# Kernel tuning notes

Measured on AMD Instinct MI355X. Metric: run time of the kernel, lower is better.

The kernel has to match this reference:

```python
import jax, jax.numpy as jnp
import numpy as np

N = 500000   # total nodes in batched graph
B = 8192     # number of graphs
H = 128      # hidden_dim
L = 3        # num_layer -> feature_dim F = H*L = 384
F = H * L
S2S_STEPS = 3
VOCAB = 143


def setup_inputs() -> dict:
    key = jax.random.key(0)
    ks = jax.random.split(key, 12)
    sc = 0.02
    unit_type = jax.random.randint(ks[0], (N,), 0, VOCAB)
    # sorted segment ids covering every graph (contiguous, all B segments non-empty)
    node2graph = (jnp.arange(N) * B) // N
    return {
        'unit_type': unit_type,
        'node2graph': node2graph,
        'embed':    jax.random.normal(ks[1], (VOCAB, H)) * sc,
        'msg_W1':   jax.random.normal(ks[2], (H, 2 * H)) * sc,
        'msg_b1':   jnp.zeros((H,)),
        'msg_W2':   jax.random.normal(ks[3], (H, H)) * sc,
        'msg_b2':   jnp.zeros((H,)),
        'gru_Wih':  jax.random.normal(ks[4], (3 * H, H)) * sc,
        'gru_Whh':  jax.random.normal(ks[5], (3 * H, H)) * sc,
        'gru_bih':  jnp.zeros((3 * H,)),
        'gru_bhh':  jnp.zeros((3 * H,)),
        'lstm_Wih': jax.random.normal(ks[6], (4 * F, 2 * F)) * sc,
        'lstm_Whh': jax.random.normal(ks[7], (4 * F, F)) * sc,
        'lstm_bih': jnp.zeros((4 * F,)),
        'lstm_bhh': jnp.zeros((4 * F,)),
    }


def _gru_step(x, h, Wih, Whh, bih, bhh):
    # single-timestep PyTorch GRU cell; gate order r, z, n
    gi = x @ Wih.T + bih
    gh = h @ Whh.T + bhh
    ir, iz, inn = jnp.split(gi, 3, axis=-1)
    hr, hz, hn = jnp.split(gh, 3, axis=-1)
    r = jax.nn.sigmoid(ir + hr)
    z = jax.nn.sigmoid(iz + hz)
    n = jnp.tanh(inn + r * hn)
    return (1.0 - z) * n + z * h


def _lstm_step(x, h, c, Wih, Whh, bih, bhh):
    # single-timestep PyTorch LSTM cell; gate order i, f, g, o
    g = x @ Wih.T + bih + h @ Whh.T + bhh
    i, f, gc, o = jnp.split(g, 4, axis=-1)
    c = jax.nn.sigmoid(f) * c + jax.nn.sigmoid(i) * jnp.tanh(gc)
    h = jax.nn.sigmoid(o) * jnp.tanh(c)
    return h, c


def reference(unit_type, node2graph, embed, msg_W1, msg_b1, msg_W2, msg_b2,
              gru_Wih, gru_Whh, gru_bih, gru_bhh,
              lstm_Wih, lstm_Whh, lstm_bih, lstm_bhh):
    # --- node update stack ---
    layer_input = embed[unit_type]          # [N, H]
    hx = layer_input                        # GRU hidden state (1 layer)
    hiddens = []
    for _ in range(L):
        x2 = jnp.concatenate([layer_input, layer_input], axis=-1)   # [N, 2H]
        msg = jnp.maximum(x2 @ msg_W1.T + msg_b1, 0.0) @ msg_W2.T + msg_b2
        hx = _gru_step(msg, hx, gru_Wih, gru_Whh, gru_bih, gru_bhh)
        hiddens.append(hx)
        layer_input = hx
    node_feature = jnp.concatenate(hiddens, axis=-1)                # [N, F]

    # --- Set2Set readout ---
    h = jnp.zeros((B, F), dtype=node_feature.dtype)
    c = jnp.zeros((B, F), dtype=node_feature.dtype)
    q_star = jnp.zeros((B, 2 * F), dtype=node_feature.dtype)
    for _ in range(S2S_STEPS):
        h, c = _lstm_step(q_star, h, c, lstm_Wih, lstm_Whh, lstm_bih, lstm_bhh)
        q = h                                                       # [B, F]
        logits = jnp.sum(q[node2graph] * node_feature, axis=-1)     # [N]
        m = jax.ops.segment_max(logits, node2graph, num_segments=B,
                                indices_are_sorted=True)
        e = jnp.exp(logits - m[node2graph])
        z = jax.ops.segment_sum(e, node2graph, num_segments=B,
                                indices_are_sorted=True)
        att = e / z[node2graph]                                     # [N]
        pooled = jax.ops.segment_sum(att[:, None] * node_feature, node2graph,
                                     num_segments=B, indices_are_sorted=True)
        q_star = jnp.concatenate([q, pooled], axis=-1)              # [B, 2F]

    return q_star, node_feature
```

## Files before the change

kernel.cpp:

```cpp
#include <hip/hip_runtime.h>

typedef unsigned short u16;
typedef unsigned int   u32;
typedef u16 bfx8 __attribute__((ext_vector_type(8)));
typedef __bf16 bf16x8 __attribute__((ext_vector_type(8)));
typedef float  f32x4  __attribute__((ext_vector_type(4)));

#define NH  128
#define NF  384
#define K2F 768
#define NG4 1536

__device__ __forceinline__ float bf2f(u16 u){ return __uint_as_float(((u32)u) << 16); }
__device__ __forceinline__ u16 f2bf(float f){
  __bf16 h = (__bf16)f;
  return __builtin_bit_cast(u16, h);
}
__device__ __forceinline__ float fsig(float x){ return 1.0f / (1.0f + __expf(-x)); }
__device__ __forceinline__ float ftanh(float x){ return 1.0f - 2.0f / (__expf(2.0f * x) + 1.0f); }

struct P {
  const int *unit_type, *n2g;
  const void *embed, *w1, *b1, *w2, *b2, *gwih, *gwhh, *gbih, *gbhh, *lwih, *lwhh, *lbih, *lbhh;
  int *flag, *segS, *segE;
  u16 *embedB;
  u16 *W1eb, *W2b, *Wihb, *Whhb;
  float *b1f, *b2f, *bihG, *bhhG;
  u16 *WcatB;
  float *bsum;
  float *h1v, *c1v;
  float *hbuf, *cbuf, *pooled;
  u16 *xcatB;
  float *gout;
  u16 *nfb;
  int useNfb;
  void *out; long qsz;
  int N, B, embedN;
};

__device__ __forceinline__ float ldin(const void* p, long i, int isbf){
  return isbf ? bf2f(((const u16*)p)[i]) : ((const float*)p)[i];
}

__global__ void k_detect(P p){
  __shared__ int cnt;
  if (threadIdx.x == 0) cnt = 0;
  __syncthreads();
  const u32* w = (const u32*)p.embed;
  const int nw = p.embedN / 2;
  int bad = 0;
  for (int i = threadIdx.x; i < nw; i += blockDim.x){
    u32 v = w[i];
    float fhi = __uint_as_float(v & 0xffff0000u);
    float flo = __uint_as_float(v << 16);
    if (!(fabsf(fhi) < 2.0f)) bad++;
    if (!(fabsf(flo) < 2.0f)) bad++;
  }
  atomicAdd(&cnt, bad);
  __syncthreads();
  if (threadIdx.x == 0) *p.flag = (cnt == 0) ? 1 : 0;
}

__global__ void k_prep(P p){
  long o = (long)blockIdx.x * 256 + threadIdx.x;
  const int isbf = *p.flag;
  if (o < p.embedN){ p.embedB[o] = f2bf(ldin(p.embed, o, isbf)); return; } o -= p.embedN;
  if (o < 16384){ long cc = o >> 7, k = o & 127;
    float v = ldin(p.w1, cc*256 + k, isbf) + ldin(p.w1, cc*256 + 128 + k, isbf);
    p.W1eb[o] = f2bf(v); return; } o -= 16384;
  if (o < 16384){ p.W2b[o]  = f2bf(ldin(p.w2, o, isbf));   return; } o -= 16384;
  if (o < 49152){ p.Wihb[o] = f2bf(ldin(p.gwih, o, isbf)); return; } o -= 49152;
  if (o < 49152){ p.Whhb[o] = f2bf(ldin(p.gwhh, o, isbf)); return; } o -= 49152;
  if (o < (long)NG4*K2F){ long j = o / K2F, k = o - j*K2F;
    float v = ldin(p.lwih, o, isbf);
    if (k < NF) v += ldin(p.lwhh, j*NF + k, isbf);
    p.WcatB[o] = f2bf(v); return; } o -= (long)NG4*K2F;
  if (o < NH){ p.b1f[o] = ldin(p.b1, o, isbf); return; } o -= NH;
  if (o < NH){ p.b2f[o] = ldin(p.b2, o, isbf); return; } o -= NH;
  if (o < NF){ p.bihG[o] = ldin(p.gbih, o, isbf); return; } o -= NF;
  if (o < NF){ p.bhhG[o] = ldin(p.gbhh, o, isbf); return; } o -= NF;
  if (o < NG4){ p.bsum[o] = ldin(p.lbih, o, isbf) + ldin(p.lbhh, o, isbf); return; } o -= NG4;
  if (o < p.B){ p.segS[o] = 0; p.segE[o] = 0; }
}

__global__ void k_segb(P p){
  int i = (int)blockIdx.x * 256 + threadIdx.x;
  if (i >= p.N) return;
  int g = p.n2g[i];
  if (g < 0 || g >= p.B) return;
  if (i == 0        || p.n2g[i-1] != g) p.segS[g] = i;
  if (i == p.N - 1  || p.n2g[i+1] != g) p.segE[g] = i + 1;
}

__device__ __forceinline__ f32x4 MF(bf16x8 a, bf16x8 b, f32x4 c){
  return __builtin_amdgcn_mfma_f32_16x16x32_bf16(a, b, c, 0, 0, 0);
}
__device__ __forceinline__ bf16x8 ldA(const u16* buf, int m0, int k0, int lane){
  const int row = m0 + (lane & 15);
  const int byte = (row*256 + (k0 + (lane>>4)*8)*2) ^ ((row&7)<<4);
  return *(const bf16x8*)((const char*)buf + byte);
}
__device__ __forceinline__ bf16x8 ldB(const u16* __restrict__ W, int n0, int k0, int lane){
  return *(const bf16x8*)(W + (long)(n0 + (lane&15))*NH + k0 + (lane>>4)*8);
}
__device__ __forceinline__ bf16x8 ldBs(const u16* __restrict__ W, long stride,
                                       int n0, int k0, int lane){
  return *(const bf16x8*)(W + (long)(n0 + (lane&15))*stride + k0 + (lane>>4)*8);
}
__device__ __forceinline__ void stLDS(u16* buf, int row, int col, float v){
  const int byte = (row*256 + col*2) ^ ((row&7)<<4);
  *(u16*)((char*)buf + byte) = f2bf(v);
}
__device__ __forceinline__ float ldLDS(const u16* buf, int row, int col){
  const int byte = (row*256 + col*2) ^ ((row&7)<<4);
  return bf2f(*(const u16*)((const char*)buf + byte));
}
__device__ __forceinline__ u16 ldLDSraw(const u16* buf, int row, int col){
  const int byte = (row*256 + col*2) ^ ((row&7)<<4);
  return *(const u16*)((const char*)buf + byte);
}

__global__ __launch_bounds__(256, 3) void k_stageA_mfma(P p){
  __shared__ u16 hA[64*128];
  __shared__ u16 mA[64*128];
  __shared__ u16 gA[64*128];
  const int t = (int)threadIdx.x;
  const int lane = t & 63, w = t >> 6;
  const int node0 = (int)blockIdx.x * 64;
  const int cL = lane & 15;
  const int isbf = *p.flag;

  {
    const int row = t >> 2, seg = t & 3;
    const int node = min(node0 + row, p.N - 1);
    int ut = p.unit_type[node];
    ut = min(max(ut, 0), p.embedN/NH - 1);
    const u16* src = p.embedB + (long)ut*NH + seg*32;
    #pragma unroll
    for (int i = 0; i < 4; ++i){
      const int col = seg*32 + i*8;
      const int byte = (row*256 + col*2) ^ ((row&7)<<4);
      *(bfx8*)((char*)hA + byte) = *(const bfx8*)(src + i*8);
    }
  }
  __syncthreads();

  u16*   out16 = (u16*)p.out;
  float* out32 = (float*)p.out;

  #pragma unroll 1
  for (int l = 0; l < 3; ++l){
    {
      f32x4 acc[2][4];
      #pragma unroll
      for (int nt = 0; nt < 2; ++nt){
        const float b = p.b1f[w*32 + nt*16 + cL];
        #pragma unroll
        for (int m = 0; m < 4; ++m) acc[nt][m] = {b,b,b,b};
      }
      for (int k0 = 0; k0 < 128; k0 += 32){
        bf16x8 bv[2];
        #pragma unroll
        for (int nt = 0; nt < 2; ++nt) bv[nt] = ldB(p.W1eb, w*32 + nt*16, k0, lane);
        bf16x8 a[4];
        #pragma unroll
        for (int m = 0; m < 4; ++m) a[m] = ldA(hA, m*16, k0, lane);
        #pragma unroll
        for (int nt = 0; nt < 2; ++nt)
          #pragma unroll
          for (int m = 0; m < 4; ++m) acc[nt][m] = MF(a[m], bv[nt], acc[nt][m]);
      }
      #pragma unroll
      for (int nt = 0; nt < 2; ++nt)
        #pragma unroll
        for (int m = 0; m < 4; ++m)
          #pragma unroll
          for (int j = 0; j < 4; ++j)
            stLDS(mA, m*16 + (lane>>4)*4 + j, w*32 + nt*16 + cL,
                  fmaxf(acc[nt][m][j], 0.0f));
    }
    __syncthreads();
    {
      f32x4 acc[2][4];
      #pragma unroll
      for (int nt = 0; nt < 2; ++nt){
        const float b = p.b2f[w*32 + nt*16 + cL];
        #pragma unroll
        for (int m = 0; m < 4; ++m) acc[nt][m] = {b,b,b,b};
      }
      for (int k0 = 0; k0 < 128; k0 += 32){
        bf16x8 bv[2];
        #pragma unroll
        for (int nt = 0; nt < 2; ++nt) bv[nt] = ldB(p.W2b, w*32 + nt*16, k0, lane);
        bf16x8 a[4];
        #pragma unroll
        for (int m = 0; m < 4; ++m) a[m] = ldA(mA, m*16, k0, lane);
        #pragma unroll
        for (int nt = 0; nt < 2; ++nt)
          #pragma unroll
          for (int m = 0; m < 4; ++m) acc[nt][m] = MF(a[m], bv[nt], acc[nt][m]);
      }
      __syncthreads();
      #pragma unroll
      for (int nt = 0; nt < 2; ++nt)
        #pragma unroll
        for (int m = 0; m < 4; ++m)
          #pragma unroll
          for (int j = 0; j < 4; ++j)
            stLDS(gA, m*16 + (lane>>4)*4 + j, w*32 + nt*16 + cL, acc[nt][m][j]);
    }
    __syncthreads();
    f32x4 rr[2][4];
    {
      f32x4 acc[4][4];
      #pragma unroll
      for (int tc = 0; tc < 4; ++tc){
        const int col = (tc < 2 ? 0 : 128) + w*32 + (tc&1)*16 + cL;
        const float b = p.bihG[col] + p.bhhG[col];
        #pragma unroll
        for (int m = 0; m < 4; ++m) acc[tc][m] = {b,b,b,b};
      }
      for (int k0 = 0; k0 < 128; k0 += 32){
        bf16x8 bv[4];
        #pragma unroll
        for (int tc = 0; tc < 4; ++tc)
          bv[tc] = ldB(p.Wihb, (tc < 2 ? 0 : 128) + w*32 + (tc&1)*16, k0, lane);
        bf16x8 a[4];
        #pragma unroll
        for (int m = 0; m < 4; ++m) a[m] = ldA(gA, m*16, k0, lane);
        #pragma unroll
        for (int tc = 0; tc < 4; ++tc)
          #pragma unroll
          for (int m = 0; m < 4; ++m) acc[tc][m] = MF(a[m], bv[tc], acc[tc][m]);
      }
      for (int k0 = 0; k0 < 128; k0 += 32){
        bf16x8 bv[4];
        #pragma unroll
        for (int tc = 0; tc < 4; ++tc)
          bv[tc] = ldB(p.Whhb, (tc < 2 ? 0 : 128) + w*32 + (tc&1)*16, k0, lane);
        bf16x8 a[4];
        #pragma unroll
        for (int m = 0; m < 4; ++m) a[m] = ldA(hA, m*16, k0, lane);
        #pragma unroll
        for (int tc = 0; tc < 4; ++tc)
          #pragma unroll
          for (int m = 0; m < 4; ++m) acc[tc][m] = MF(a[m], bv[tc], acc[tc][m]);
      }
      #pragma unroll
      for (int nt = 0; nt < 2; ++nt)
        #pragma unroll
        for (int m = 0; m < 4; ++m)
          #pragma unroll
          for (int j = 0; j < 4; ++j){
            rr[nt][m][j] = fsig(acc[nt][m][j]);
            stLDS(mA, m*16 + (lane>>4)*4 + j, w*32 + nt*16 + cL,
                  fsig(acc[nt+2][m][j]));
          }
    }
    {
      f32x4 inn[2][4], hnn[2][4];
      #pragma unroll
      for (int nt = 0; nt < 2; ++nt){
        const int col = 256 + w*32 + nt*16 + cL;
        const float bi = p.bihG[col], bh = p.bhhG[col];
        #pragma unroll
        for (int m = 0; m < 4; ++m){ inn[nt][m] = {bi,bi,bi,bi}; hnn[nt][m] = {bh,bh,bh,bh}; }
      }
      for (int k0 = 0; k0 < 128; k0 += 32){
        bf16x8 bv[2];
        #pragma unroll
        for (int nt = 0; nt < 2; ++nt) bv[nt] = ldB(p.Wihb, 256 + w*32 + nt*16, k0, lane);
        bf16x8 a[4];
        #pragma unroll
        for (int m = 0; m < 4; ++m) a[m] = ldA(gA, m*16, k0, lane);
        #pragma unroll
        for (int nt = 0; nt < 2; ++nt)
          #pragma unroll
          for (int m = 0; m < 4; ++m) inn[nt][m] = MF(a[m], bv[nt], inn[nt][m]);
      }
      for (int k0 = 0; k0 < 128; k0 += 32){
        bf16x8 bv[2];
        #pragma unroll
        for (int nt = 0; nt < 2; ++nt) bv[nt] = ldB(p.Whhb, 256 + w*32 + nt*16, k0, lane);
        bf16x8 a[4];
        #pragma unroll
        for (int m = 0; m < 4; ++m) a[m] = ldA(hA, m*16, k0, lane);
        #pragma unroll
        for (int nt = 0; nt < 2; ++nt)
          #pragma unroll
          for (int m = 0; m < 4; ++m) hnn[nt][m] = MF(a[m], bv[nt], hnn[nt][m]);
      }
      #pragma unroll
      for (int nt = 0; nt < 2; ++nt)
        #pragma unroll
        for (int m = 0; m < 4; ++m)
          #pragma unroll
          for (int j = 0; j < 4; ++j){
            const int row = m*16 + (lane>>4)*4 + j;
            const int col = w*32 + nt*16 + cL;
            const float nn = ftanh(fmaf(rr[nt][m][j], hnn[nt][m][j], inn[nt][m][j]));
            const float zv = ldLDS(mA, row, col);
            const float hv = ldLDS(hA, row, col);
            inn[nt][m][j] = fmaf(zv, hv - nn, nn);
          }
      __syncthreads();
      #pragma unroll
      for (int nt = 0; nt < 2; ++nt)
        #pragma unroll
        for (int m = 0; m < 4; ++m)
          #pragma unroll
          for (int j = 0; j < 4; ++j)
            stLDS(hA, m*16 + (lane>>4)*4 + j, w*32 + nt*16 + cL, inn[nt][m][j]);
      __syncthreads();
    }
    {
      const int col = t & 127;
      const int rh  = t >> 7;
      #pragma unroll 4
      for (int rb = 0; rb < 64; rb += 2){
        const int row = rb + rh;
        const int node = node0 + row;
        if (node < p.N){
          const u16 hv16 = ldLDSraw(hA, row, col);
          const long fi = (long)node*NF + l*NH + col;
          if (isbf){
            __builtin_nontemporal_store(hv16, &out16[p.qsz + fi]);
          } else {
            __builtin_nontemporal_store(bf2f(hv16), &out32[p.qsz + fi]);
            if (p.useNfb) __builtin_nontemporal_store(hv16, &p.nfb[fi]);
          }
        }
      }
    }
  }
}

__global__ void k_lstm0(P p){
  const int d = (int)threadIdx.x;
  if (d >= NF) return;
  const float i_ = fsig(p.bsum[d]);
  const float gc = ftanh(p.bsum[2*NF + d]);
  const float o_ = fsig(p.bsum[3*NF + d]);
  const float cn = i_ * gc;
  p.c1v[d] = cn;
  p.h1v[d] = o_ * ftanh(cn);
}

__global__ __launch_bounds__(256) void k_attn(P p, const float* __restrict__ qsrc,
                                              int qstride, int finalstep){
  __shared__ alignas(16) char raw[32 * NF * 4];
  __shared__ float qs[NF];
  __shared__ float att[32];
  __shared__ float sM, sZ, sSc;

  u16*   nb = (u16*)raw;
  float* nfl = (float*)raw;
  const int t = (int)threadIdx.x;
  const int g = (int)blockIdx.x;
  const int isbf = *p.flag;
  const int bftile = isbf | p.useNfb;
  const u16* nbase = isbf ? (const u16*)p.out + p.qsz : p.nfb;
  const float* o32 = (const float*)p.out;

  for (int i = t; i < NF; i += 256) qs[i] = qsrc[(long)g*qstride + i];
  if (t == 0){ sM = -1e30f; sZ = 0.0f; sSc = 1.0f; }
  int n0 = p.segS[g], n1 = p.segE[g];
  n0 = max(n0, 0); n1 = min(n1, p.N);
  float acc0 = 0.f, acc1 = 0.f;
  __syncthreads();

  for (int base = n0; base < n1; base += 32){
    const int cnt = min(32, n1 - base);
    {
      const int i = t >> 3, q8 = t & 7;
      if (i < cnt){
        if (bftile){
          const bfx8* src = (const bfx8*)(nbase + (long)(base + i)*NF + q8*48);
          #pragma unroll
          for (int j8 = 0; j8 < 6; ++j8)
            *(bfx8*)&nb[i*NF + q8*48 + j8*8] = __builtin_nontemporal_load(src + j8);
        } else {
          const f32x4* src = (const f32x4*)(o32 + p.qsz + (long)(base + i)*NF + q8*48);
          #pragma unroll
          for (int j4 = 0; j4 < 12; ++j4)
            *(f32x4*)&nfl[i*NF + q8*48 + j4*4] = __builtin_nontemporal_load(src + j4);
        }
      }
    }
    __syncthreads();
    {
      const int w = t >> 6, lane = t & 63;
      for (int ii = w; ii < cnt; ii += 4){
        float dot = 0.f;
        #pragma unroll
        for (int j = 0; j < 6; ++j){
          const int d = lane + 64*j;
          const float v = bftile ? bf2f(nb[ii*NF + d]) : nfl[ii*NF + d];
          dot = fmaf(v, qs[d], dot);
        }
        #pragma unroll
        for (int off = 32; off; off >>= 1) dot += __shfl_xor(dot, off);
        if (lane == 0) att[ii] = dot;
      }
    }
    __syncthreads();
    if (t < 32){
      const float l = (t < cnt) ? att[t] : -1e30f;
      float m = l;
      #pragma unroll
      for (int off = 16; off; off >>= 1) m = fmaxf(m, __shfl_xor(m, off));
      const float mnew = fmaxf(sM, m);
      const float e = (t < cnt) ? __expf(l - mnew) : 0.f;
      float z = e;
      #pragma unroll
      for (int off = 16; off; off >>= 1) z += __shfl_xor(z, off);
      if (t < cnt) att[t] = e;
      if (t == 0){
        const float sc = __expf(sM - mnew);
        sSc = sc; sZ = sZ * sc + z; sM = mnew;
      }
    }
    __syncthreads();
    {
      const float sc = sSc;
      acc0 *= sc; acc1 *= sc;
      for (int ii = 0; ii < cnt; ++ii){
        const float a = att[ii];
        const float v0 = bftile ? bf2f(nb[ii*NF + t]) : nfl[ii*NF + t];
        acc0 = fmaf(a, v0, acc0);
        if (t < 128){
          const float v1 = bftile ? bf2f(nb[ii*NF + 256 + t]) : nfl[ii*NF + 256 + t];
          acc1 = fmaf(a, v1, acc1);
        }
      }
    }
    __syncthreads();
  }

  const float invZ = (sZ != 0.0f) ? 1.0f / sZ : 0.0f;
  const float p0 = acc0 * invZ, p1 = acc1 * invZ;
  p.pooled[(long)g*NF + t] = p0;
  if (t < 128) p.pooled[(long)g*NF + 256 + t] = p1;
  if (finalstep){
    const long rb = (long)g * K2F;
    if (isbf){
      u16* o = (u16*)p.out;
      o[rb + t] = f2bf(qs[t]);
      if (t < 128) o[rb + 256 + t] = f2bf(qs[256 + t]);
      o[rb + NF + t] = f2bf(p0);
      if (t < 128) o[rb + NF + 256 + t] = f2bf(p1);
    } else {
      float* o = (float*)p.out;
      o[rb + t] = qs[t];
      if (t < 128) o[rb + 256 + t] = qs[256 + t];
      o[rb + NF + t] = p0;
      if (t < 128) o[rb + NF + 256 + t] = p1;
    }
  }
}

__global__ void k_xcat(P p, const float* __restrict__ hsrc, int hstride){
  const int d2 = (int)blockIdx.x * 256 + threadIdx.x;
  const int g  = (int)blockIdx.y;
  if (d2 >= K2F) return;
  const float v = (d2 < NF) ? hsrc[(long)g*hstride + d2]
                            : p.pooled[(long)g*NF + d2 - NF];
  p.xcatB[(long)g*K2F + d2] = f2bf(v);
}

__global__ __launch_bounds__(256, 4) void k_gemm_mfma(P p){
  __shared__ u16 aT[64*128];
  const int t = (int)threadIdx.x;
  const int lane = t & 63, w = t >> 6, cL = lane & 15;
  const int row0 = (int)blockIdx.x * 64, col0 = (int)blockIdx.y * 128;

  f32x4 acc[2][4];
  #pragma unroll
  for (int nt = 0; nt < 2; ++nt)
    #pragma unroll
    for (int m = 0; m < 4; ++m) acc[nt][m] = {0.f,0.f,0.f,0.f};

  for (int kc = 0; kc < K2F; kc += 128){
    __syncthreads();
    {
      const int row = t >> 2, seg = t & 3;
      const int gr = row0 + row;
      const u16* src = p.xcatB + (long)gr*K2F + kc + seg*32;
      #pragma unroll
      for (int i = 0; i < 4; ++i){
        const int col = seg*32 + i*8;
        const int byte = (row*256 + col*2) ^ ((row&7)<<4);
        bfx8 v = {0,0,0,0,0,0,0,0};
        if (gr < p.B) v = *(const bfx8*)(src + i*8);
        *(bfx8*)((char*)aT + byte) = v;
      }
    }
    __syncthreads();
    for (int k0 = 0; k0 < 128; k0 += 32){
      bf16x8 bv[2];
      #pragma unroll
      for (int nt = 0; nt < 2; ++nt)
        bv[nt] = ldBs(p.WcatB, K2F, col0 + w*32 + nt*16, kc + k0, lane);
      bf16x8 a[4];
      #pragma unroll
      for (int m = 0; m < 4; ++m) a[m] = ldA(aT, m*16, k0, lane);
      #pragma unroll
      for (int nt = 0; nt < 2; ++nt)
        #pragma unroll
        for (int m = 0; m < 4; ++m) acc[nt][m] = MF(a[m], bv[nt], acc[nt][m]);
    }
  }
  #pragma unroll
  for (int nt = 0; nt < 2; ++nt){
    const int col = col0 + w*32 + nt*16 + cL;
    const float bs = p.bsum[col];
    #pragma unroll
    for (int m = 0; m < 4; ++m)
      #pragma unroll
      for (int j = 0; j < 4; ++j){
        const int row = row0 + m*16 + (lane>>4)*4 + j;
        if (row < p.B) p.gout[(long)row*NG4 + col] = acc[nt][m][j] + bs;
      }
  }
}

__global__ void k_gates(P p, const float* __restrict__ csrc, int cstride){
  const long idx = (long)blockIdx.x * 256 + threadIdx.x;
  if (idx >= (long)p.B * NF) return;
  const int g = (int)(idx / NF), d = (int)(idx - (long)g*NF);
  const float* gr = p.gout + (long)g*NG4;
  const float i_ = fsig(gr[d]);
  const float f_ = fsig(gr[NF + d]);
  const float gc = ftanh(gr[2*NF + d]);
  const float o_ = fsig(gr[3*NF + d]);
  const float cp = csrc[(long)g*cstride + d];
  const float cn = fmaf(f_, cp, i_ * gc);
  p.cbuf[(long)g*NF + d] = cn;
  p.hbuf[(long)g*NF + d] = o_ * ftanh(cn);
}

extern "C" void kernel_launch(void* const* d_in, const int* in_sizes, int n_in,
                              void* d_out, int out_size, void* d_ws, size_t ws_size,
                              hipStream_t stream){
  P p{};
  p.unit_type = (const int*)d_in[0];
  p.n2g  = (const int*)d_in[1];
  p.embed = d_in[2];  p.w1 = d_in[3];  p.b1 = d_in[4];  p.w2 = d_in[5];  p.b2 = d_in[6];
  p.gwih = d_in[7];  p.gwhh = d_in[8]; p.gbih = d_in[9]; p.gbhh = d_in[10];
  p.lwih = d_in[11]; p.lwhh = d_in[12]; p.lbih = d_in[13]; p.lbhh = d_in[14];

  const int N = in_sizes[0];
  const int B = (int)(((long)out_size - (long)N*NF) / K2F);
  p.N = N; p.B = B; p.embedN = in_sizes[2];
  p.out = d_out; p.qsz = (long)B * K2F;

  char* w = (char*)d_ws;
  size_t used = 0;
  auto alloc = [&](size_t bytes) -> char* {
    char* r = w + used;
    used += (bytes + 255) & ~(size_t)255;
    return r;
  };
  p.flag  = (int*)alloc(4);
  p.segS  = (int*)alloc((size_t)B*4);
  p.segE  = (int*)alloc((size_t)B*4);
  p.embedB= (u16*)  alloc((size_t)p.embedN*2);
  p.W1eb  = (u16*)  alloc(16384*2);
  p.W2b   = (u16*)  alloc(16384*2);
  p.Wihb  = (u16*)  alloc(49152*2);
  p.Whhb  = (u16*)  alloc(49152*2);
  p.b1f   = (float*)alloc(NH*4);
  p.b2f   = (float*)alloc(NH*4);
  p.bihG  = (float*)alloc(NF*4);
  p.bhhG  = (float*)alloc(NF*4);
  p.WcatB = (u16*)  alloc((size_t)NG4*K2F*2);
  p.bsum  = (float*)alloc(NG4*4);
  p.h1v   = (float*)alloc(NF*4);
  p.c1v   = (float*)alloc(NF*4);
  p.hbuf  = (float*)alloc((size_t)B*NF*4);
  p.cbuf  = (float*)alloc((size_t)B*NF*4);
  p.pooled= (float*)alloc((size_t)B*NF*4);
  p.xcatB = (u16*)  alloc((size_t)B*K2F*2);
  p.gout  = (float*)alloc((size_t)B*NG4*4);
  if (used > ws_size){
    (void)hipMemsetAsync(d_out, 0, (size_t)out_size * 2, stream);
    return;
  }
  const size_t nfbBytes = (size_t)N * NF * 2;
  if (used + nfbBytes + 256 <= ws_size){
    p.nfb = (u16*)alloc(nfbBytes);
    p.useNfb = 1;
  } else {
    p.nfb = (u16*)p.flag;
    p.useNfb = 0;
  }

  const long prepTot = (long)p.embedN + 16384 + 16384 + 49152 + 49152
                     + (long)NG4*K2F + NH + NH + NF + NF + NG4 + B;

  k_detect<<<1, 256, 0, stream>>>(p);
  k_prep  <<<(int)((prepTot + 255)/256), 256, 0, stream>>>(p);
  k_segb  <<<(N + 255)/256, 256, 0, stream>>>(p);
  k_stageA_mfma<<<(N + 63)/64, 256, 0, stream>>>(p);
  k_lstm0 <<<1, NF, 0, stream>>>(p);

  const dim3 gemmG((B + 63)/64, NG4/128);
  k_attn <<<B, 256, 0, stream>>>(p, p.h1v, 0, 0);
  k_xcat <<<dim3(3, B), 256, 0, stream>>>(p, p.h1v, 0);
  k_gemm_mfma<<<gemmG, 256, 0, stream>>>(p);
  k_gates<<<(int)(((long)B*NF + 255)/256), 256, 0, stream>>>(p, p.c1v, 0);
  k_attn <<<B, 256, 0, stream>>>(p, p.hbuf, NF, 0);
  k_xcat <<<dim3(3, B), 256, 0, stream>>>(p, p.hbuf, NF);
  k_gemm_mfma<<<gemmG, 256, 0, stream>>>(p);
  k_gates<<<(int)(((long)B*NF + 255)/256), 256, 0, stream>>>(p, p.cbuf, NF);
  k_attn <<<B, 256, 0, stream>>>(p, p.hbuf, NF, 1);
}
```

Measured before the change: 1.994 ms.

## Give each wave its own 16-row slab and fuse GRU gates without block syncs

Stage A is reorganised so that each wave owns 16 node rows and computes all 128 output columns of every matmul. The A fragments stay in registers, so no block-wide __syncthreads are needed. The GRU r/z/n gate matmuls and their elementwise update are fused into one per-column-tile loop, and the two LDS buffers ping-pong across layers, cutting LDS from 48KB to 32KB per block. In exchange, every wave now fetches the full weight matrices (four times the weight traffic per block), and the column-tile loops are not unrolled, which shortens the independent MFMA chains.

```diff
diff --git a/kernel.cpp b/kernel.cpp
--- a/kernel.cpp
+++ b/kernel.cpp
@@ -121,17 +121,21 @@
 }
 
 __global__ __launch_bounds__(256, 3) void k_stageA_mfma(P p){
-  __shared__ u16 hA[64*128];
-  __shared__ u16 mA[64*128];
-  __shared__ u16 gA[64*128];
+  __shared__ u16 bufA[64*128];
+  __shared__ u16 bufB[64*128];
   const int t = (int)threadIdx.x;
   const int lane = t & 63, w = t >> 6;
   const int node0 = (int)blockIdx.x * 64;
+  const int r0 = w * 16;
   const int cL = lane & 15;
   const int isbf = *p.flag;
 
+  u16* bufH = bufA;
+  u16* bufM = bufB;
+
   {
-    const int row = t >> 2, seg = t & 3;
+    const int row = r0 + (lane >> 2);
+    const int seg = lane & 3;
     const int node = min(node0 + row, p.N - 1);
     int ut = p.unit_type[node];
     ut = min(max(ut, 0), p.embedN/NH - 1);
@@ -140,198 +144,107 @@
     for (int i = 0; i < 4; ++i){
       const int col = seg*32 + i*8;
       const int byte = (row*256 + col*2) ^ ((row&7)<<4);
-      *(bfx8*)((char*)hA + byte) = *(const bfx8*)(src + i*8);
-    }
-  }
-  __syncthreads();
+      *(bfx8*)((char*)bufH + byte) = *(const bfx8*)(src + i*8);
+    }
+  }
 
   u16*   out16 = (u16*)p.out;
   float* out32 = (float*)p.out;
 
   #pragma unroll 1
   for (int l = 0; l < 3; ++l){
+    bf16x8 ah[4];
+    #pragma unroll
+    for (int k = 0; k < 4; ++k) ah[k] = ldA(bufH, r0, k*32, lane);
+
+    #pragma unroll 1
+    for (int ct = 0; ct < 8; ++ct){
+      const float b = p.b1f[ct*16 + cL];
+      f32x4 acc = {b,b,b,b};
+      #pragma unroll
+      for (int k = 0; k < 4; ++k){
+        const bf16x8 bv = ldB(p.W1eb, ct*16, k*32, lane);
+        acc = MF(ah[k], bv, acc);
+      }
+      #pragma unroll
+      for (int j = 0; j < 4; ++j)
+        stLDS(bufM, r0 + (lane>>4)*4 + j, ct*16 + cL, fmaxf(acc[j], 0.0f));
+    }
     {
-      f32x4 acc[2][4];
-      #pragma unroll
-      for (int nt = 0; nt < 2; ++nt){
-        const float b = p.b1f[w*32 + nt*16 + cL];
-        #pragma unroll
-        for (int m = 0; m < 4; ++m) acc[nt][m] = {b,b,b,b};
-      }
-      for (int k0 = 0; k0 < 128; k0 += 32){
-        bf16x8 bv[2];
-        #pragma unroll
-        for (int nt = 0; nt < 2; ++nt) bv[nt] = ldB(p.W1eb, w*32 + nt*16, k0, lane);
-        bf16x8 a[4];
-        #pragma unroll
-        for (int m = 0; m < 4; ++m) a[m] = ldA(hA, m*16, k0, lane);
-        #pragma unroll
-        for (int nt = 0; nt < 2; ++nt)
-          #pragma unroll
-          for (int m = 0; m < 4; ++m) acc[nt][m] = MF(a[m], bv[nt], acc[nt][m]);
-      }
-      #pragma unroll
-      for (int nt = 0; nt < 2; ++nt)
-        #pragma unroll
-        for (int m = 0; m < 4; ++m)
-          #pragma unroll
-          for (int j = 0; j < 4; ++j)
-            stLDS(mA, m*16 + (lane>>4)*4 + j, w*32 + nt*16 + cL,
-                  fmaxf(acc[nt][m][j], 0.0f));
-    }
-    __syncthreads();
+      bf16x8 am[4];
+      #pragma unroll
+      for (int k = 0; k < 4; ++k) am[k] = ldA(bufM, r0, k*32, lane);
+      #pragma unroll 1
+      for (int ct = 0; ct < 8; ++ct){
+        const float b = p.b2f[ct*16 + cL];
+        f32x4 acc = {b,b,b,b};
+        #pragma unroll
+        for (int k = 0; k < 4; ++k){
+          const bf16x8 bv = ldB(p.W2b, ct*16, k*32, lane);
+          acc = MF(am[k], bv, acc);
+        }
+        #pragma unroll
+        for (int j = 0; j < 4; ++j)
+          stLDS(bufM, r0 + (lane>>4)*4 + j, ct*16 + cL, acc[j]);
+      }
+    }
     {
-      f32x4 acc[2][4];
-      #pragma unroll
-      for (int nt = 0; nt < 2; ++nt){
-        const float b = p.b2f[w*32 + nt*16 + cL];
-        #pragma unroll
-        for (int m = 0; m < 4; ++m) acc[nt][m] = {b,b,b,b};
-      }
-      for (int k0 = 0; k0 < 128; k0 += 32){
-        bf16x8 bv[2];
-        #pragma unroll
-        for (int nt = 0; nt < 2; ++nt) bv[nt] = ldB(p.W2b, w*32 + nt*16, k0, lane);
-        bf16x8 a[4];
-        #pragma unroll
-        for (int m = 0; m < 4; ++m) a[m] = ldA(mA, m*16, k0, lane);
-        #pragma unroll
-        for (int nt = 0; nt < 2; ++nt)
-          #pragma unroll
-          for (int m = 0; m < 4; ++m) acc[nt][m] = MF(a[m], bv[nt], acc[nt][m]);
-      }
-      __syncthreads();
-      #pragma unroll
-      for (int nt = 0; nt < 2; ++nt)
-        #pragma unroll
-        for (int m = 0; m < 4; ++m)
-          #pragma unroll
-          for (int j = 0; j < 4; ++j)
-            stLDS(gA, m*16 + (lane>>4)*4 + j, w*32 + nt*16 + cL, acc[nt][m][j]);
-    }
-    __syncthreads();
-    f32x4 rr[2][4];
-    {
-      f32x4 acc[4][4];
-      #pragma unroll
-      for (int tc = 0; tc < 4; ++tc){
-        const int col = (tc < 2 ? 0 : 128) + w*32 + (tc&1)*16 + cL;
-        const float b = p.bihG[col] + p.bhhG[col];
-        #pragma unroll
-        for (int m = 0; m < 4; ++m) acc[tc][m] = {b,b,b,b};
-      }
-      for (int k0 = 0; k0 < 128; k0 += 32){
-        bf16x8 bv[4];
-        #pragma unroll
-        for (int tc = 0; tc < 4; ++tc)
-          bv[tc] = ldB(p.Wihb, (tc < 2 ? 0 : 128) + w*32 + (tc&1)*16, k0, lane);
-        bf16x8 a[4];
-        #pragma unroll
-        for (int m = 0; m < 4; ++m) a[m] = ldA(gA, m*16, k0, lane);
-        #pragma unroll
-        for (int tc = 0; tc < 4; ++tc)
-          #pragma unroll
-          for (int m = 0; m < 4; ++m) acc[tc][m] = MF(a[m], bv[tc], acc[tc][m]);
-      }
-      for (int k0 = 0; k0 < 128; k0 += 32){
-        bf16x8 bv[4];
-        #pragma unroll
-        for (int tc = 0; tc < 4; ++tc)
-          bv[tc] = ldB(p.Whhb, (tc < 2 ? 0 : 128) + w*32 + (tc&1)*16, k0, lane);
-        bf16x8 a[4];
-        #pragma unroll
-        for (int m = 0; m < 4; ++m) a[m] = ldA(hA, m*16, k0, lane);
-        #pragma unroll
-        for (int tc = 0; tc < 4; ++tc)
-          #pragma unroll
-          for (int m = 0; m < 4; ++m) acc[tc][m] = MF(a[m], bv[tc], acc[tc][m]);
-      }
-      #pragma unroll
-      for (int nt = 0; nt < 2; ++nt)
-        #pragma unroll
-        for (int m = 0; m < 4; ++m)
-          #pragma unroll
-          for (int j = 0; j < 4; ++j){
-            rr[nt][m][j] = fsig(acc[nt][m][j]);
-            stLDS(mA, m*16 + (lane>>4)*4 + j, w*32 + nt*16 + cL,
-                  fsig(acc[nt+2][m][j]));
+      bf16x8 am[4];
+      #pragma unroll
+      for (int k = 0; k < 4; ++k) am[k] = ldA(bufM, r0, k*32, lane);
+      #pragma unroll 1
+      for (int ct = 0; ct < 8; ++ct){
+        const int c16 = ct*16 + cL;
+        const float br = p.bihG[c16]       + p.bhhG[c16];
+        const float bz = p.bihG[128 + c16] + p.bhhG[128 + c16];
+        const float bi = p.bihG[256 + c16];
+        const float bh = p.bhhG[256 + c16];
+        f32x4 ar = {br,br,br,br}, az = {bz,bz,bz,bz};
+        f32x4 ai = {bi,bi,bi,bi}, an = {bh,bh,bh,bh};
+        #pragma unroll
+        for (int k = 0; k < 4; ++k){
+          bf16x8 bv;
+          bv = ldB(p.Wihb,       ct*16, k*32, lane); ar = MF(am[k], bv, ar);
+          bv = ldB(p.Whhb,       ct*16, k*32, lane); ar = MF(ah[k], bv, ar);
+          bv = ldB(p.Wihb, 128 + ct*16, k*32, lane); az = MF(am[k], bv, az);
+          bv = ldB(p.Whhb, 128 + ct*16, k*32, lane); az = MF(ah[k], bv, az);
+          bv = ldB(p.Wihb, 256 + ct*16, k*32, lane); ai = MF(am[k], bv, ai);
+          bv = ldB(p.Whhb, 256 + ct*16, k*32, lane); an = MF(ah[k], bv, an);
+        }
+        #pragma unroll
+        for (int j = 0; j < 4; ++j){
+          const int row = r0 + (lane>>4)*4 + j;
+          const int col = ct*16 + cL;
+          const float r = fsig(ar[j]);
+          const float z = fsig(az[j]);
+          const float nn = ftanh(fmaf(r, an[j], ai[j]));
+          const float hv = ldLDS(bufH, row, col);
+          stLDS(bufM, row, col, fmaf(z, hv - nn, nn));
+        }
+      }
+    }
+    #pragma unroll 1
+    for (int rj = 0; rj < 16; ++rj){
+      const int row = r0 + rj;
+      const int node = node0 + row;
+      if (node < p.N){
+        const u16 va = ldLDSraw(bufM, row, lane);
+        const u16 vb = ldLDSraw(bufM, row, 64 + lane);
+        const long fi = (long)node*NF + l*NH;
+        if (isbf){
+          __builtin_nontemporal_store(va, &out16[p.qsz + fi + lane]);
+          __builtin_nontemporal_store(vb, &out16[p.qsz + fi + 64 + lane]);
+        } else {
+          __builtin_nontemporal_store(bf2f(va), &out32[p.qsz + fi + lane]);
+          __builtin_nontemporal_store(bf2f(vb), &out32[p.qsz + fi + 64 + lane]);
+          if (p.useNfb){
+            __builtin_nontemporal_store(va, &p.nfb[fi + lane]);
+            __builtin_nontemporal_store(vb, &p.nfb[fi + 64 + lane]);
           }
-    }
-    {
-      f32x4 inn[2][4], hnn[2][4];
-      #pragma unroll
-      for (int nt = 0; nt < 2; ++nt){
-        const int col = 256 + w*32 + nt*16 + cL;
-        const float bi = p.bihG[col], bh = p.bhhG[col];
-        #pragma unroll
-        for (int m = 0; m < 4; ++m){ inn[nt][m] = {bi,bi,bi,bi}; hnn[nt][m] = {bh,bh,bh,bh}; }
-      }
-      for (int k0 = 0; k0 < 128; k0 += 32){
-        bf16x8 bv[2];
-        #pragma unroll
-        for (int nt = 0; nt < 2; ++nt) bv[nt] = ldB(p.Wihb, 256 + w*32 + nt*16, k0, lane);
-        bf16x8 a[4];
-        #pragma unroll
-        for (int m = 0; m < 4; ++m) a[m] = ldA(gA, m*16, k0, lane);
-        #pragma unroll
-        for (int nt = 0; nt < 2; ++nt)
-          #pragma unroll
-          for (int m = 0; m < 4; ++m) inn[nt][m] = MF(a[m], bv[nt], inn[nt][m]);
-      }
-      for (int k0 = 0; k0 < 128; k0 += 32){
-        bf16x8 bv[2];
-        #pragma unroll
-        for (int nt = 0; nt < 2; ++nt) bv[nt] = ldB(p.Whhb, 256 + w*32 + nt*16, k0, lane);
-        bf16x8 a[4];
-        #pragma unroll
-        for (int m = 0; m < 4; ++m) a[m] = ldA(hA, m*16, k0, lane);
-        #pragma unroll
-        for (int nt = 0; nt < 2; ++nt)
-          #pragma unroll
-          for (int m = 0; m < 4; ++m) hnn[nt][m] = MF(a[m], bv[nt], hnn[nt][m]);
-      }
-      #pragma unroll
-      for (int nt = 0; nt < 2; ++nt)
-        #pragma unroll
-        for (int m = 0; m < 4; ++m)
-          #pragma unroll
-          for (int j = 0; j < 4; ++j){
-            const int row = m*16 + (lane>>4)*4 + j;
-            const int col = w*32 + nt*16 + cL;
-            const float nn = ftanh(fmaf(rr[nt][m][j], hnn[nt][m][j], inn[nt][m][j]));
-            const float zv = ldLDS(mA, row, col);
-            const float hv = ldLDS(hA, row, col);
-            inn[nt][m][j] = fmaf(zv, hv - nn, nn);
-          }
-      __syncthreads();
-      #pragma unroll
-      for (int nt = 0; nt < 2; ++nt)
-        #pragma unroll
-        for (int m = 0; m < 4; ++m)
-          #pragma unroll
-          for (int j = 0; j < 4; ++j)
-            stLDS(hA, m*16 + (lane>>4)*4 + j, w*32 + nt*16 + cL, inn[nt][m][j]);
-      __syncthreads();
-    }
-    {
-      const int col = t & 127;
-      const int rh  = t >> 7;
-      #pragma unroll 4
-      for (int rb = 0; rb < 64; rb += 2){
-        const int row = rb + rh;
-        const int node = node0 + row;
-        if (node < p.N){
-          const u16 hv16 = ldLDSraw(hA, row, col);
-          const long fi = (long)node*NF + l*NH + col;
-          if (isbf){
-            __builtin_nontemporal_store(hv16, &out16[p.qsz + fi]);
-          } else {
-            __builtin_nontemporal_store(bf2f(hv16), &out32[p.qsz + fi]);
-            if (p.useNfb) __builtin_nontemporal_store(hv16, &p.nfb[fi]);
-          }
-        }
-      }
-    }
+        }
+      }
+    }
+    u16* tmp = bufH; bufH = bufM; bufM = tmp;
   }
 }
 
```

After: 3.265 ms. 63.8% more time.
